# Kernel optimization log

Hardware: AMD Instinct MI355X
Metric: run time of the kernel (lower is better)

## Reference

```python
import jax, jax.numpy as jnp
import numpy as np

INPUT_DIM = 8192
HIDDEN = 128
STEPS = 4096


def _uniform(key, shape, fan_in, dtype=jnp.float32):
    lim = 1.0 / np.sqrt(fan_in)
    return jax.random.uniform(key, shape, dtype, minval=-lim, maxval=lim)


def setup_inputs() -> dict:
    key = jax.random.key(0)
    ks = jax.random.split(key, 10)
    x0 = jax.random.normal(ks[0], (INPUT_DIM,), jnp.float32)
    # encoder Linear(input_dim -> hidden)
    W_enc = _uniform(ks[1], (HIDDEN, INPUT_DIM), INPUT_DIM)
    b_enc = _uniform(ks[2], (HIDDEN,), INPUT_DIM)
    # GRUCell(hidden -> hidden): weight_ih (3H, H), weight_hh (3H, H), bias (3H,), bias_n (H,)
    W_ih = _uniform(ks[3], (3 * HIDDEN, HIDDEN), HIDDEN)
    W_hh = _uniform(ks[4], (3 * HIDDEN, HIDDEN), HIDDEN)
    bias = _uniform(ks[5], (3 * HIDDEN,), HIDDEN)
    bias_n = _uniform(ks[6], (HIDDEN,), HIDDEN)
    # decoder Linear(hidden -> input_dim)
    W_dec = _uniform(ks[7], (INPUT_DIM, HIDDEN), HIDDEN)
    b_dec = _uniform(ks[8], (INPUT_DIM,), HIDDEN)
    return {"x0": x0, "W_enc": W_enc, "b_enc": b_enc, "W_ih": W_ih,
            "W_hh": W_hh, "bias": bias, "bias_n": bias_n,
            "W_dec": W_dec, "b_dec": b_dec, "steps": STEPS}


def reference(x0, W_enc, b_enc, W_ih, W_hh, bias, bias_n, W_dec, b_dec, steps):
    H = W_hh.shape[1]
    h0 = jnp.zeros((H,), x0.dtype)

    def scan_step(carry, _):
        h, x_prev = carry
        e = W_enc @ x_prev + b_enc                       # encoder: [H]
        ig = W_ih @ e + bias                             # [3H]
        hg = W_hh @ h                                    # [3H]
        ir, iz, i_n = jnp.split(ig, 3)
        hr, hz, hn = jnp.split(hg, 3)
        r = jax.nn.sigmoid(ir + hr)                      # reset gate
        z = jax.nn.sigmoid(iz + hz)                      # update gate
        n = jnp.tanh(i_n + r * (hn + bias_n))            # candidate
        h_new = n + z * (h - n)                          # equinox GRUCell update
        x_next = W_dec @ h_new + b_dec                   # decoder: [input_dim]
        return (h_new, x_next), x_next

    _, predictions = jax.lax.scan(scan_step, (h0, x0), None, length=steps)
    return predictions
```

## Files before the change

### kernel.cpp

```cpp
#include <hip/hip_runtime.h>
#include <math.h>

#define IN_DIM 8192
#define HID 128
#define NSTEPS 4096

typedef _Float16 f16x8 __attribute__((ext_vector_type(8)));
typedef float f32x4 __attribute__((ext_vector_type(4)));

__device__ __forceinline__ float sigm(float x) { return 1.f / (1.f + __expf(-x)); }
__device__ __forceinline__ float tanh_f(float x) {
    x = fminf(fmaxf(x, -15.f), 15.f);
    float e = __expf(2.f * x);
    return (e - 1.f) / (e + 1.f);
}

__global__ __launch_bounds__(128) void k_precompute_M(
    const float* __restrict__ W_enc, const float* __restrict__ W_dec,
    const float* __restrict__ b_enc, const float* __restrict__ b_dec,
    const float* __restrict__ x0,
    float* __restrict__ M, float* __restrict__ cvec, float* __restrict__ e1)
{
    const int p = blockIdx.x;
    const int t = threadIdx.x;
    __shared__ float wl[128];
    __shared__ float red[256];
    float m0 = 0.f, m1 = 0.f, m2 = 0.f, m3 = 0.f, cacc = 0.f, eacc = 0.f;
    for (int i0 = 0; i0 < IN_DIM; i0 += 128) {
        float w = W_enc[(size_t)p * IN_DIM + i0 + t];
        cacc = fmaf(w, b_dec[i0 + t], cacc);
        eacc = fmaf(w, x0[i0 + t], eacc);
        wl[t] = w;
        __syncthreads();
#pragma unroll 8
        for (int k = 0; k < 128; k += 4) {
            m0 = fmaf(wl[k],     W_dec[(size_t)(i0 + k) * HID + t], m0);
            m1 = fmaf(wl[k + 1], W_dec[(size_t)(i0 + k + 1) * HID + t], m1);
            m2 = fmaf(wl[k + 2], W_dec[(size_t)(i0 + k + 2) * HID + t], m2);
            m3 = fmaf(wl[k + 3], W_dec[(size_t)(i0 + k + 3) * HID + t], m3);
        }
        __syncthreads();
    }
    M[p * HID + t] = (m0 + m1) + (m2 + m3);
    red[t] = cacc; red[128 + t] = eacc;
    __syncthreads();
    for (int s = 64; s > 0; s >>= 1) {
        if (t < s) { red[t] += red[t + s]; red[128 + t] += red[128 + t + s]; }
        __syncthreads();
    }
    if (t == 0) { cvec[p] = red[0] + b_enc[p]; e1[p] = red[128] + b_enc[p]; }
}

__global__ __launch_bounds__(128) void k_precompute_G(
    const float* __restrict__ W_ih, const float* __restrict__ W_hh,
    const float* __restrict__ bias, const float* __restrict__ M,
    const float* __restrict__ cvec, const float* __restrict__ e1,
    float* __restrict__ G, float* __restrict__ gb, float* __restrict__ ig1)
{
    const int r = blockIdx.x;
    const int q = threadIdx.x;
    if (r >= 384) {
        G[(size_t)r * HID + q] = W_hh[(size_t)(r - 384) * HID + q];
        if (q == 0) gb[r] = 0.f;
        return;
    }
    __shared__ float red[256];
    float a0 = 0.f, a1 = 0.f, a2 = 0.f, a3 = 0.f;
#pragma unroll 8
    for (int k = 0; k < HID; k += 4) {
        a0 = fmaf(W_ih[r * HID + k],     M[(k) * HID + q], a0);
        a1 = fmaf(W_ih[r * HID + k + 1], M[(k + 1) * HID + q], a1);
        a2 = fmaf(W_ih[r * HID + k + 2], M[(k + 2) * HID + q], a2);
        a3 = fmaf(W_ih[r * HID + k + 3], M[(k + 3) * HID + q], a3);
    }
    G[(size_t)r * HID + q] = (a0 + a1) + (a2 + a3);
    float wq = W_ih[r * HID + q];
    red[q] = wq * cvec[q];
    red[128 + q] = wq * e1[q];
    __syncthreads();
    for (int s = 64; s > 0; s >>= 1) {
        if (q < s) { red[q] += red[q + s]; red[128 + q] += red[128 + q + s]; }
        __syncthreads();
    }
    if (q == 0) { gb[r] = red[0] + bias[r]; ig1[r] = red[128] + bias[r]; }
}

__global__ __launch_bounds__(256) void k_pack(
    const float* __restrict__ G, _Float16* __restrict__ Gp)
{
    int id = blockIdx.x * 256 + threadIdx.x;
    int i = id & 7;
    int l = (id >> 3) & 63;
    int frag = id >> 9;
    int c = frag & 3;
    int b = (frag >> 2) % 6;
    int w = frag / 24;
    int row = 128 * b + 16 * w + (l & 15);
    int k = 32 * c + ((l >> 4) << 3) + i;
    Gp[id] = (_Float16)G[row * HID + k];
}

#define WF24(F) F(0,0) F(0,1) F(0,2) F(0,3) F(1,0) F(1,1) F(1,2) F(1,3) \
                F(2,0) F(2,1) F(2,2) F(2,3) F(3,0) F(3,1) F(3,2) F(3,3) \
                F(4,0) F(4,1) F(4,2) F(4,3) F(5,0) F(5,1) F(5,2) F(5,3)

__global__ __launch_bounds__(512, 2) void k_recurrence(
    const _Float16* __restrict__ Gp, const float* __restrict__ gb,
    const float* __restrict__ ig1, const float* __restrict__ bias_n,
    float* __restrict__ H)
{
    const int t = threadIdx.x;
    const int l = t & 63;
    const int w = t >> 6;
    __shared__ _Float16 hbuf[2][HID];

    const f16x8* gpb = (const f16x8*)Gp;
#define DECLW(b,c) f16x8 wf##b##c = gpb[(w * 24 + b * 4 + c) * 64 + l];
    WF24(DECLW)
#undef DECLW
#define PINW(b,c) asm volatile("" : "+a"(wf##b##c));
    WF24(PINW)
#undef PINW

    const int g4 = l >> 4;
    const int ul = 16 * w + 4 * g4 + (l & 3);
    const bool writer = (l & 12) == 0;

    const float gb0 = gb[ul];
    const float gb1 = gb[HID + ul];
    const float gb2 = gb[2 * HID + ul];
    const float bnr = bias_n[ul];
    const f32x4 zero = {0.f, 0.f, 0.f, 0.f};

    float hp;

    {
        float i0 = ig1[ul], i1 = ig1[HID + ul], i2 = ig1[2 * HID + ul];
        float zg = sigm(i1);
        float ng = tanh_f(fmaf(sigm(i0), bnr, i2));
        hp = ng - zg * ng;
        if (writer) {
            hbuf[1][ul] = (_Float16)hp;
            H[ul] = hp;
        }
    }
    __syncthreads();

    const bool sel0 = (l & 1) != 0;
    const bool sel1 = (l & 2) != 0;

    for (int st = 1; st < NSTEPS; ++st) {
        const char* cb = (const char*)&hbuf[st & 1][0];
        f16x8 b0 = *(const f16x8*)(cb + 16 * g4);
        f16x8 b1 = *(const f16x8*)(cb + 16 * g4 + 64);
        f16x8 b2 = *(const f16x8*)(cb + 16 * g4 + 128);
        f16x8 b3 = *(const f16x8*)(cb + 16 * g4 + 192);
        f32x4 d0 = __builtin_amdgcn_mfma_f32_16x16x32_f16(wf00, b0, zero, 0, 0, 0);
        f32x4 d1 = __builtin_amdgcn_mfma_f32_16x16x32_f16(wf10, b0, zero, 0, 0, 0);
        f32x4 d2 = __builtin_amdgcn_mfma_f32_16x16x32_f16(wf20, b0, zero, 0, 0, 0);
        f32x4 d3 = __builtin_amdgcn_mfma_f32_16x16x32_f16(wf30, b0, zero, 0, 0, 0);
        f32x4 d4 = __builtin_amdgcn_mfma_f32_16x16x32_f16(wf40, b0, zero, 0, 0, 0);
        f32x4 d5 = __builtin_amdgcn_mfma_f32_16x16x32_f16(wf50, b0, zero, 0, 0, 0);
        d0 = __builtin_amdgcn_mfma_f32_16x16x32_f16(wf01, b1, d0, 0, 0, 0);
        d1 = __builtin_amdgcn_mfma_f32_16x16x32_f16(wf11, b1, d1, 0, 0, 0);
        d2 = __builtin_amdgcn_mfma_f32_16x16x32_f16(wf21, b1, d2, 0, 0, 0);
        d3 = __builtin_amdgcn_mfma_f32_16x16x32_f16(wf31, b1, d3, 0, 0, 0);
        d4 = __builtin_amdgcn_mfma_f32_16x16x32_f16(wf41, b1, d4, 0, 0, 0);
        d5 = __builtin_amdgcn_mfma_f32_16x16x32_f16(wf51, b1, d5, 0, 0, 0);
        d0 = __builtin_amdgcn_mfma_f32_16x16x32_f16(wf02, b2, d0, 0, 0, 0);
        d1 = __builtin_amdgcn_mfma_f32_16x16x32_f16(wf12, b2, d1, 0, 0, 0);
        d2 = __builtin_amdgcn_mfma_f32_16x16x32_f16(wf22, b2, d2, 0, 0, 0);
        d3 = __builtin_amdgcn_mfma_f32_16x16x32_f16(wf32, b2, d3, 0, 0, 0);
        d4 = __builtin_amdgcn_mfma_f32_16x16x32_f16(wf42, b2, d4, 0, 0, 0);
        d5 = __builtin_amdgcn_mfma_f32_16x16x32_f16(wf52, b2, d5, 0, 0, 0);
        d0 = __builtin_amdgcn_mfma_f32_16x16x32_f16(wf03, b3, d0, 0, 0, 0);
        d1 = __builtin_amdgcn_mfma_f32_16x16x32_f16(wf13, b3, d1, 0, 0, 0);
        d2 = __builtin_amdgcn_mfma_f32_16x16x32_f16(wf23, b3, d2, 0, 0, 0);
        d3 = __builtin_amdgcn_mfma_f32_16x16x32_f16(wf33, b3, d3, 0, 0, 0);
        d4 = __builtin_amdgcn_mfma_f32_16x16x32_f16(wf43, b3, d4, 0, 0, 0);
        d5 = __builtin_amdgcn_mfma_f32_16x16x32_f16(wf53, b3, d5, 0, 0, 0);
#define SEL(b, e) { float s01 = sel0 ? d##b[1] : d##b[0]; \
                    float s23 = sel0 ? d##b[3] : d##b[2]; \
                    e = sel1 ? s23 : s01; }
        float e0, e1, e2, e3, e4, e5;
        SEL(0, e0) SEL(1, e1) SEL(2, e2) SEL(3, e3) SEL(4, e4) SEL(5, e5)
#undef SEL
        float rg = sigm(e0 + gb0 + e3);
        float zg = sigm(e1 + gb1 + e4);
        float ng = tanh_f(e2 + gb2 + rg * (e5 + bnr));
        hp = ng + zg * (hp - ng);
        if (writer) {
            hbuf[(st + 1) & 1][ul] = (_Float16)hp;
            H[(size_t)st * HID + ul] = hp;
        }
        __syncthreads();
    }
}

__global__ __launch_bounds__(256) void k_decode(
    const float* __restrict__ H, const float* __restrict__ W_dec,
    const float* __restrict__ b_dec, float* __restrict__ out)
{
    __shared__ float4 As[64 * 32];
    __shared__ float4 Bs[64 * 32];
    const int tid = threadIdx.x;
    const int t0 = blockIdx.y * 64;
    const int i0 = blockIdx.x * 64;
#pragma unroll 8
    for (int j = 0; j < 8; ++j) {
        int f = tid + 256 * j;
        int t = f >> 5;
        int k4 = f & 31;
        int sw = k4 ^ (t & 7);
        As[t * 32 + sw] = *(const float4*)(H + (size_t)(t0 + t) * HID + 4 * k4);
        Bs[t * 32 + sw] = *(const float4*)(W_dec + (size_t)(i0 + t) * HID + 4 * k4);
    }
    __syncthreads();
    const int tx = tid & 15, ty = tid >> 4;
    const int xa = ty & 7, xb = tx & 7;
    float acc[4][4] = {{0.f}};
#pragma unroll 8
    for (int k4 = 0; k4 < 32; ++k4) {
        float4 a[4], b[4];
        int ia = k4 ^ xa, ib = k4 ^ xb;
#pragma unroll
        for (int u = 0; u < 4; ++u) a[u] = As[(ty + 16 * u) * 32 + ia];
#pragma unroll
        for (int v = 0; v < 4; ++v) b[v] = Bs[(tx + 16 * v) * 32 + ib];
#pragma unroll
        for (int u = 0; u < 4; ++u)
#pragma unroll
            for (int v = 0; v < 4; ++v) {
                acc[u][v] = fmaf(a[u].x, b[v].x, acc[u][v]);
                acc[u][v] = fmaf(a[u].y, b[v].y, acc[u][v]);
                acc[u][v] = fmaf(a[u].z, b[v].z, acc[u][v]);
                acc[u][v] = fmaf(a[u].w, b[v].w, acc[u][v]);
            }
    }
#pragma unroll
    for (int u = 0; u < 4; ++u) {
        int t = t0 + ty + 16 * u;
#pragma unroll
        for (int v = 0; v < 4; ++v) {
            int i = i0 + tx + 16 * v;
            out[(size_t)t * IN_DIM + i] = acc[u][v] + b_dec[i];
        }
    }
}

extern "C" void kernel_launch(void* const* d_in, const int* in_sizes, int n_in,
                              void* d_out, int out_size, void* d_ws, size_t ws_size,
                              hipStream_t stream)
{
    const float* x0     = (const float*)d_in[0];
    const float* W_enc  = (const float*)d_in[1];
    const float* b_enc  = (const float*)d_in[2];
    const float* W_ih   = (const float*)d_in[3];
    const float* W_hh   = (const float*)d_in[4];
    const float* bias   = (const float*)d_in[5];
    const float* bias_n = (const float*)d_in[6];
    const float* W_dec  = (const float*)d_in[7];
    const float* b_dec  = (const float*)d_in[8];
    float* out = (float*)d_out;

    float* ws   = (float*)d_ws;
    float* M    = ws;
    float* cvec = ws + 16384;
    float* e1   = ws + 16512;
    float* ig1  = ws + 16640;
    float* gb   = ws + 17024;
    float* G    = ws + 17792;
    float* H    = ws + 116096;
    _Float16* Gp = (_Float16*)(ws + 640384);

    k_precompute_M<<<128, 128, 0, stream>>>(W_enc, W_dec, b_enc, b_dec, x0, M, cvec, e1);
    k_precompute_G<<<768, 128, 0, stream>>>(W_ih, W_hh, bias, M, cvec, e1, G, gb, ig1);
    k_pack<<<384, 256, 0, stream>>>(G, Gp);
    k_recurrence<<<1, 512, 0, stream>>>(Gp, gb, ig1, bias_n, H);
    dim3 grid(IN_DIM / 64, NSTEPS / 64);
    k_decode<<<grid, 256, 0, stream>>>(H, W_dec, b_dec, out);
}
```

Baseline: 2.984 ms.

## Compute decoder GEMM with fp16 MFMA directly from global memory

Replaces the LDS-tiled fp32 FMA decoder GEMM with per-wavefront 16x16x32 fp16 MFMA instructions. Operands are loaded straight from global memory and converted to fp16 in registers, so the shared-memory staging and the barrier go away. This trades fp32 accuracy for fp16 inputs with fp32 accumulation. The decoder is a 4096x8192x128 GEMM, but total time is likely dominated by the sequential GRU recurrence, which limits the overall gain.

New measurement: 2.970 ms. Within noise of the previous version (-0.5%).

```diff
diff --git a/kernel.cpp b/kernel.cpp
--- a/kernel.cpp
+++ b/kernel.cpp
@@ -201,51 +201,70 @@
     const float* __restrict__ H, const float* __restrict__ W_dec,
     const float* __restrict__ b_dec, float* __restrict__ out)
 {
-    __shared__ float4 As[64 * 32];
-    __shared__ float4 Bs[64 * 32];
     const int tid = threadIdx.x;
-    const int t0 = blockIdx.y * 64;
+    const int l = tid & 63;
+    const int w = tid >> 6;
+    const int t0 = blockIdx.y * 64 + 16 * w;
     const int i0 = blockIdx.x * 64;
-#pragma unroll 8
-    for (int j = 0; j < 8; ++j) {
-        int f = tid + 256 * j;
-        int t = f >> 5;
-        int k4 = f & 31;
-        int sw = k4 ^ (t & 7);
-        As[t * 32 + sw] = *(const float4*)(H + (size_t)(t0 + t) * HID + 4 * k4);
-        Bs[t * 32 + sw] = *(const float4*)(W_dec + (size_t)(i0 + t) * HID + 4 * k4);
-    }
-    __syncthreads();
-    const int tx = tid & 15, ty = tid >> 4;
-    const int xa = ty & 7, xb = tx & 7;
-    float acc[4][4] = {{0.f}};
-#pragma unroll 8
-    for (int k4 = 0; k4 < 32; ++k4) {
-        float4 a[4], b[4];
-        int ia = k4 ^ xa, ib = k4 ^ xb;
+    const int r = l & 15;
+    const int g = l >> 4;
+
+    f32x4 acc0 = {0.f, 0.f, 0.f, 0.f};
+    f32x4 acc1 = {0.f, 0.f, 0.f, 0.f};
+    f32x4 acc2 = {0.f, 0.f, 0.f, 0.f};
+    f32x4 acc3 = {0.f, 0.f, 0.f, 0.f};
+
+#define CVT8(dst, lo, hi) f16x8 dst; \
+    dst[0] = (_Float16)lo.x; dst[1] = (_Float16)lo.y; \
+    dst[2] = (_Float16)lo.z; dst[3] = (_Float16)lo.w; \
+    dst[4] = (_Float16)hi.x; dst[5] = (_Float16)hi.y; \
+    dst[6] = (_Float16)hi.z; dst[7] = (_Float16)hi.w;
+
 #pragma unroll
-        for (int u = 0; u < 4; ++u) a[u] = As[(ty + 16 * u) * 32 + ia];
-#pragma unroll
-        for (int v = 0; v < 4; ++v) b[v] = Bs[(tx + 16 * v) * 32 + ib];
-#pragma unroll
-        for (int u = 0; u < 4; ++u)
-#pragma unroll
-            for (int v = 0; v < 4; ++v) {
-                acc[u][v] = fmaf(a[u].x, b[v].x, acc[u][v]);
-                acc[u][v] = fmaf(a[u].y, b[v].y, acc[u][v]);
-                acc[u][v] = fmaf(a[u].z, b[v].z, acc[u][v]);
-                acc[u][v] = fmaf(a[u].w, b[v].w, acc[u][v]);
-            }
-    }
-#pragma unroll
-    for (int u = 0; u < 4; ++u) {
-        int t = t0 + ty + 16 * u;
-#pragma unroll
-        for (int v = 0; v < 4; ++v) {
-            int i = i0 + tx + 16 * v;
-            out[(size_t)t * IN_DIM + i] = acc[u][v] + b_dec[i];
-        }
-    }
+    for (int c = 0; c < 4; ++c) {
+        const float* ap = H + (size_t)(t0 + r) * HID + 32 * c + 8 * g;
+        float4 alo = *(const float4*)ap;
+        float4 ahi = *(const float4*)(ap + 4);
+        CVT8(af, alo, ahi)
+        const float* bp0 = W_dec + (size_t)(i0 + r) * HID + 32 * c + 8 * g;
+        {
+            float4 blo = *(const float4*)bp0;
+            float4 bhi = *(const float4*)(bp0 + 4);
+            CVT8(bf, blo, bhi)
+            acc0 = __builtin_amdgcn_mfma_f32_16x16x32_f16(af, bf, acc0, 0, 0, 0);
+        }
+        {
+            const float* bp = bp0 + (size_t)16 * HID;
+            float4 blo = *(const float4*)bp;
+            float4 bhi = *(const float4*)(bp + 4);
+            CVT8(bf, blo, bhi)
+            acc1 = __builtin_amdgcn_mfma_f32_16x16x32_f16(af, bf, acc1, 0, 0, 0);
+        }
+        {
+            const float* bp = bp0 + (size_t)32 * HID;
+            float4 blo = *(const float4*)bp;
+            float4 bhi = *(const float4*)(bp + 4);
+            CVT8(bf, blo, bhi)
+            acc2 = __builtin_amdgcn_mfma_f32_16x16x32_f16(af, bf, acc2, 0, 0, 0);
+        }
+        {
+            const float* bp = bp0 + (size_t)48 * HID;
+            float4 blo = *(const float4*)bp;
+            float4 bhi = *(const float4*)(bp + 4);
+            CVT8(bf, blo, bhi)
+            acc3 = __builtin_amdgcn_mfma_f32_16x16x32_f16(af, bf, acc3, 0, 0, 0);
+        }
+    }
+#undef CVT8
+
+#define EPI(ct, acc) { \
+        float bd = b_dec[i0 + 16 * ct + r]; \
+        out[(size_t)(t0 + 4 * g + 0) * IN_DIM + i0 + 16 * ct + r] = acc[0] + bd; \
+        out[(size_t)(t0 + 4 * g + 1) * IN_DIM + i0 + 16 * ct + r] = acc[1] + bd; \
+        out[(size_t)(t0 + 4 * g + 2) * IN_DIM + i0 + 16 * ct + r] = acc[2] + bd; \
+        out[(size_t)(t0 + 4 * g + 3) * IN_DIM + i0 + 16 * ct + r] = acc[3] + bd; }
+    EPI(0, acc0) EPI(1, acc1) EPI(2, acc2) EPI(3, acc3)
+#undef EPI
 }
 
 extern "C" void kernel_launch(void* const* d_in, const int* in_sizes, int n_in,
```
